# Kernel tuning notes

Measured on AMD Instinct MI355X. Metric: run time of the kernel, lower is better.

The kernel has to match this reference:

```python
import jax, jax.numpy as jnp
import numpy as np

M = 128      # max_child_num
H = 256      # hidden_size
F = 256      # node_feat_size (must equal H per original view logic)
T = 4        # edge_type_num
I = 2        # num_iterations
NSEM = 57    # Tree.num_sem


def setup_inputs() -> dict:
    key = jax.random.key(0)
    ks = jax.random.split(key, 16)
    def lin(k, shape, fan_in):
        return (jax.random.normal(k, shape, jnp.float32) / np.sqrt(fan_in)).astype(jnp.float32)
    return {
        "parent_feature": jax.random.normal(ks[0], (1, F), jnp.float32),
        "W_parent": lin(ks[1], (F, H * M), F),
        "b_parent": jnp.zeros((H * M,), jnp.float32),
        "W_exists": lin(ks[2], (H, 1), H),
        "b_exists": jnp.zeros((1,), jnp.float32),
        "W_edge_latent": lin(ks[3], (2 * H, H), 2 * H),
        "b_edge_latent": jnp.zeros((H,), jnp.float32),
        "W_edge_exists": lin(ks[4], (T, H), H),   # per-type 1-out linear, stacked
        "b_edge_exists": jnp.zeros((T,), jnp.float32),
        "W_op": lin(ks[5], (I, 3 * H + T, H), 3 * H + T),
        "b_op": jnp.zeros((I, H), jnp.float32),
        "W_child": lin(ks[6], (H * (I + 1), H), H * (I + 1)),
        "b_child": jnp.zeros((H,), jnp.float32),
        "W_sem": lin(ks[7], (H, NSEM), H),
        "b_sem": jnp.zeros((NSEM,), jnp.float32),
        "W_child2": lin(ks[8], (H, F), H),
        "b_child2": jnp.zeros((F,), jnp.float32),
    }


def reference(parent_feature, W_parent, b_parent, W_exists, b_exists,
              W_edge_latent, b_edge_latent, W_edge_exists, b_edge_exists,
              W_op, b_op, W_child, b_child, W_sem, b_sem, W_child2, b_child2):
    # parent -> per-child latents [M, H]
    cf = jax.nn.relu(parent_feature @ W_parent + b_parent).reshape(M, H)
    child_exists_logits = cf @ W_exists + b_exists                      # [M, 1]

    # pairwise edge latents [M, M, H]
    pair = jnp.concatenate([
        jnp.broadcast_to(cf[:, None, :], (M, M, H)),
        jnp.broadcast_to(cf[None, :, :], (M, M, H)),
    ], axis=-1)
    el = jax.nn.relu(pair @ W_edge_latent + b_edge_latent)              # [M, M, H]
    ee = jnp.einsum('ijh,th->ijt', el, W_edge_exists) + b_edge_exists   # [M, M, T]

    # dense-mask equivalent of torch.nonzero edge list: an edge exists per
    # (i, j, type) triple where its logit > 0 and both endpoints exist.
    exists = child_exists_logits[:, 0] > 0                              # [M]
    mask = (ee > 0) & exists[:, None, None] & exists[None, :, None]     # [M, M, T]
    maskf = mask.astype(cf.dtype)

    iter_feats = [cf]
    for i in range(I):
        # node_edge_op input is concat([cf_src, cf_dst, edge_latent, onehot(t)*logit]);
        # split the linear into per-block matmuls to avoid a [M,M,T,3H+T] concat.
        W1, W2, W3, W4 = (W_op[i, :H], W_op[i, H:2 * H],
                          W_op[i, 2 * H:3 * H], W_op[i, 3 * H:])        # W4: [T, H]
        pre = ((cf @ W1)[:, None, None, :]
               + (cf @ W2)[None, :, None, :]
               + (el @ W3)[:, :, None, :]
               + ee[:, :, :, None] * W4[None, None, :, :]
               + b_op[i])                                               # [M, M, T, H]
        h = jax.nn.relu(pre) * maskf[..., None]
        # scatter_max over source index i with zero-initialized output:
        # relu output >= 0 and masked-out edges are 0, so plain max matches.
        cf = jnp.max(h, axis=(1, 2))                                    # [M, H]
        iter_feats.append(cf)

    allf = jnp.concatenate(iter_feats, axis=1)                          # [M, H*(I+1)]
    ch = jax.nn.relu(allf @ W_child + b_child)                          # [M, H]
    child_sem_logits = ch @ W_sem + b_sem                               # [M, NSEM]
    child_feats = jax.nn.relu(ch @ W_child2 + b_child2)                 # [M, F]

    return (child_feats[None], child_sem_logits[None],
            child_exists_logits[None], ee[None])
```

## Files before the change

### kernel.cpp

```cpp
#include <hip/hip_runtime.h>
#include <hip/hip_bf16.h>

#define M_ 128
#define H_ 256
#define F_ 256
#define T_ 4
#define NSEM_ 57

typedef __attribute__((ext_vector_type(8))) short bf16x8;
typedef __attribute__((ext_vector_type(4))) float f32x4;

__device__ __forceinline__ float4 ld4(const float* p) { return *reinterpret_cast<const float4*>(p); }
__device__ __forceinline__ void st4(float* p, float4 v) { *reinterpret_cast<float4*>(p) = v; }
__device__ __forceinline__ float4 add4(float4 a, float4 b) { return make_float4(a.x+b.x, a.y+b.y, a.z+b.z, a.w+b.w); }
__device__ __forceinline__ float4 relu4(float4 a) { return make_float4(fmaxf(a.x,0.f), fmaxf(a.y,0.f), fmaxf(a.z,0.f), fmaxf(a.w,0.f)); }
__device__ __forceinline__ float4 fma4(float s, float4 w, float4 c) { return make_float4(fmaf(s,w.x,c.x), fmaf(s,w.y,c.y), fmaf(s,w.z,c.z), fmaf(s,w.w,c.w)); }

__device__ __forceinline__ unsigned short f2bfu(float x) {
  unsigned u = __float_as_uint(x);
  return (unsigned short)((u + 0x7FFFu + ((u >> 16) & 1u)) >> 16);
}
__device__ __forceinline__ unsigned pack2(float lo, float hi) {
  return (unsigned)f2bfu(lo) | ((unsigned)f2bfu(hi) << 16);
}

__global__ void __launch_bounds__(256) k_parent(
    const float* __restrict__ pf, const float* __restrict__ Wp,
    const float* __restrict__ Wop, float* __restrict__ part,
    unsigned short* __restrict__ W36F, unsigned short* __restrict__ W768F)
{
  const int cb = (blockIdx.x & 31) * 1024 + threadIdx.x * 4;
  const int kc = blockIdx.x >> 5;
  __shared__ float spf[8];
  if (threadIdx.x < 8) spf[threadIdx.x] = pf[kc * 8 + threadIdx.x];
  __syncthreads();
  const float* w = Wp + (size_t)kc * 8 * 32768 + cb;
  float4 acc = make_float4(0.f, 0.f, 0.f, 0.f);
  #pragma unroll
  for (int k = 0; k < 8; ++k)
    acc = fma4(spf[k], ld4(w + (size_t)k * 32768), acc);
  st4(&part[kc * 32768 + cb], acc);

  const int g = blockIdx.x * 256 + threadIdx.x;
  if (g < 65536) {
    const int fb = g >> 9, e = g & 511;
    const int kk = fb >> 4, ct = fb & 15;
    const int l = e >> 3, q = e & 7;
    const int k = kk * 32 + ((l >> 4) << 3) + q;
    const int h = ct * 16 + (l & 15);
    W36F[g] = f2bfu(Wop[(size_t)(512 + k) * 256 + h]);
  } else {
    const int g2 = g - 65536;
    const int fb = g2 >> 9, e = g2 & 511;
    const int kk = fb >> 4, ct = fb & 15;
    const int l = e >> 3, q = e & 7;
    const int k = kk * 32 + ((l >> 4) << 3) + q;
    const int h = ct * 16 + (l & 15);
    const int row = (k < 256) ? 512 + k : (k < 512 ? k : k - 512);
    W768F[g2] = f2bfu(Wop[197632 + (size_t)row * 256 + h]);
  }
}

__global__ void __launch_bounds__(256) k_stage1(
    const float* __restrict__ part, const float* __restrict__ bp,
    const float* __restrict__ Wel, const float* __restrict__ Wop0,
    const float* __restrict__ Wex, const float* __restrict__ bex,
    float* __restrict__ cf0, float* __restrict__ A, float* __restrict__ B,
    float* __restrict__ a1, float* __restrict__ a2,
    float* __restrict__ cf1, float* __restrict__ cf2,
    float* __restrict__ out_ex)
{
  const int m = blockIdx.x >> 1, sel = blockIdx.x & 1;
  const int t = threadIdx.x;
  __shared__ float sall[256];
  __shared__ float red[2][4][256];
  __shared__ float redE[4];

  (sel ? cf2 : cf1)[m * 256 + t] = 0.f;

  float v = bp[m * 256 + t];
  #pragma unroll 8
  for (int q = 0; q < 32; ++q) v += part[q * 32768 + m * 256 + t];
  v = fmaxf(v, 0.f);
  sall[t] = v;
  if (sel == 0) {
    cf0[m * 256 + t] = v;
    float p = v * Wex[t];
    #pragma unroll
    for (int off = 32; off > 0; off >>= 1) p += __shfl_xor(p, off);
    if ((t & 63) == 0) redE[t >> 6] = p;
  }
  __syncthreads();

  const float* W0 = Wel  + (sel ? 65536 : 0);
  const float* W1 = Wop0 + (sel ? 65536 : 0);
  const int hq = (t & 63) << 2, kg = t >> 6, k0 = kg * 64;
  float4 acc0 = make_float4(0.f, 0.f, 0.f, 0.f), acc1 = acc0;
  #pragma unroll 4
  for (int k = k0; k < k0 + 64; ++k) {
    const float s = sall[k];
    acc0 = fma4(s, ld4(W0 + k * 256 + hq), acc0);
    acc1 = fma4(s, ld4(W1 + k * 256 + hq), acc1);
  }
  st4(&red[0][kg][hq], acc0);
  st4(&red[1][kg][hq], acc1);
  __syncthreads();
  if (kg < 2) {
    float4 r = add4(add4(ld4(&red[kg][0][hq]), ld4(&red[kg][1][hq])),
                    add4(ld4(&red[kg][2][hq]), ld4(&red[kg][3][hq])));
    float* dst = (kg == 0) ? (sel ? B : A) : (sel ? a2 : a1);
    st4(&dst[m * 256 + hq], r);
  }
  if (sel == 0 && t == 0)
    out_ex[m] = redE[0] + redE[1] + redE[2] + redE[3] + bex[0];
}

__global__ void __launch_bounds__(512) k_gemm0(
    const float* __restrict__ Arow, const float* __restrict__ Brow,
    const float* __restrict__ bel, const unsigned short* __restrict__ W36F,
    const float* __restrict__ Wee, const float* __restrict__ bee,
    const float* __restrict__ a1, const float* __restrict__ a2,
    const float* __restrict__ Wop0, const float* __restrict__ bop0,
    const float* __restrict__ exlog,
    float* __restrict__ ee_g, float* __restrict__ cf1)
{
  const int i  = blockIdx.x >> 2;
  const int jq = blockIdx.x & 3;
  const int t  = threadIdx.x;
  const int w  = t >> 6;
  const int l  = t & 63;
  __shared__ char sEL[32 * 512];
  __shared__ float see[32][4];
  __shared__ float sexf[32];

  const bool exi = exlog[i] > 0.f;

  {
    const int row = t >> 4;
    const int sub = t & 15;
    const int kb  = sub * 16;
    const float* Ap  = Arow + i * 256 + kb;
    const float* Bp  = Brow + (jq * 32 + row) * 256 + kb;
    const float* blp = bel + kb;
    float e[16];
    #pragma unroll
    for (int q = 0; q < 16; q += 4) {
      float4 av = ld4(Ap + q), bv = ld4(Bp + q), lv = ld4(blp + q);
      e[q+0] = fmaxf(av.x + bv.x + lv.x, 0.f);
      e[q+1] = fmaxf(av.y + bv.y + lv.y, 0.f);
      e[q+2] = fmaxf(av.z + bv.z + lv.z, 0.f);
      e[q+3] = fmaxf(av.w + bv.w + lv.w, 0.f);
    }
    float s[4] = {0.f, 0.f, 0.f, 0.f};
    #pragma unroll
    for (int tt = 0; tt < 4; ++tt) {
      #pragma unroll
      for (int q = 0; q < 16; q += 4) {
        float4 wv = ld4(Wee + tt * 256 + kb + q);
        s[tt] = fmaf(e[q+0], wv.x, s[tt]);
        s[tt] = fmaf(e[q+1], wv.y, s[tt]);
        s[tt] = fmaf(e[q+2], wv.z, s[tt]);
        s[tt] = fmaf(e[q+3], wv.w, s[tt]);
      }
    }
    #pragma unroll
    for (int off = 1; off < 16; off <<= 1) {
      s[0] += __shfl_xor(s[0], off);
      s[1] += __shfl_xor(s[1], off);
      s[2] += __shfl_xor(s[2], off);
      s[3] += __shfl_xor(s[3], off);
    }
    if (sub < 4) {
      const float v = s[sub] + bee[sub];
      see[row][sub] = v;
      ee_g[(i * 128 + jq * 32 + row) * 4 + sub] = v;
    }
    const int swz = (row & 7) << 4;
    uint4 w0, w1;
    w0.x = pack2(e[0], e[1]);  w0.y = pack2(e[2], e[3]);
    w0.z = pack2(e[4], e[5]);  w0.w = pack2(e[6], e[7]);
    w1.x = pack2(e[8], e[9]);  w1.y = pack2(e[10], e[11]);
    w1.z = pack2(e[12], e[13]); w1.w = pack2(e[14], e[15]);
    *reinterpret_cast<uint4*>(sEL + ((row * 512 + kb * 2)      ^ swz)) = w0;
    *reinterpret_cast<uint4*>(sEL + ((row * 512 + kb * 2 + 16) ^ swz)) = w1;
  }
  if (t < 32) sexf[t] = exlog[jq * 32 + t];
  __syncthreads();

  const int lr = l & 15, lk = l >> 4;
  f32x4 acc[2][2];
  #pragma unroll
  for (int jt = 0; jt < 2; ++jt)
    #pragma unroll
    for (int ct = 0; ct < 2; ++ct)
      acc[jt][ct] = (f32x4){0.f, 0.f, 0.f, 0.f};

  for (int kc = 0; kc < 8; ++kc) {
    const int kbyte = kc * 64 + lk * 16;
    bf16x8 af0 = *reinterpret_cast<const bf16x8*>(
        sEL + ((lr * 512 + kbyte) ^ ((lr & 7) << 4)));
    bf16x8 af1 = *reinterpret_cast<const bf16x8*>(
        sEL + (((16 + lr) * 512 + kbyte) ^ ((lr & 7) << 4)));
    #pragma unroll
    for (int ct = 0; ct < 2; ++ct) {
      const int fb = kc * 16 + (w * 2 + ct);
      bf16x8 bf = *reinterpret_cast<const bf16x8*>(W36F + fb * 512 + l * 8);
      acc[0][ct] = __builtin_amdgcn_mfma_f32_16x16x32_bf16(af0, bf, acc[0][ct], 0, 0, 0);
      acc[1][ct] = __builtin_amdgcn_mfma_f32_16x16x32_bf16(af1, bf, acc[1][ct], 0, 0, 0);
    }
  }

  const int c0 = w * 32 + lr, c1 = c0 + 16;
  const float b10 = a1[i * 256 + c0] + bop0[c0];
  const float b11 = a1[i * 256 + c1] + bop0[c1];
  float w40[4], w41[4];
  #pragma unroll
  for (int tt = 0; tt < 4; ++tt) {
    w40[tt] = Wop0[(768 + tt) * 256 + c0];
    w41[tt] = Wop0[(768 + tt) * 256 + c1];
  }
  float am0 = 0.f, am1 = 0.f;
  #pragma unroll
  for (int jt = 0; jt < 2; ++jt) {
    #pragma unroll
    for (int q = 0; q < 4; ++q) {
      const int jrow = jt * 16 + lk * 4 + q;
      const int j = jq * 32 + jrow;
      if (exi && (sexf[jrow] > 0.f)) {
        const float e0 = see[jrow][0], e1 = see[jrow][1];
        const float e2 = see[jrow][2], e3 = see[jrow][3];
        const float pb0 = b10 + a2[j * 256 + c0] + acc[jt][0][q];
        const float pb1 = b11 + a2[j * 256 + c1] + acc[jt][1][q];
        if (e0 > 0.f) { am0 = fmaxf(am0, fmaxf(fmaf(e0, w40[0], pb0), 0.f));
                        am1 = fmaxf(am1, fmaxf(fmaf(e0, w41[0], pb1), 0.f)); }
        if (e1 > 0.f) { am0 = fmaxf(am0, fmaxf(fmaf(e1, w40[1], pb0), 0.f));
                        am1 = fmaxf(am1, fmaxf(fmaf(e1, w41[1], pb1), 0.f)); }
        if (e2 > 0.f) { am0 = fmaxf(am0, fmaxf(fmaf(e2, w40[2], pb0), 0.f));
                        am1 = fmaxf(am1, fmaxf(fmaf(e2, w41[2], pb1), 0.f)); }
        if (e3 > 0.f) { am0 = fmaxf(am0, fmaxf(fmaf(e3, w40[3], pb0), 0.f));
                        am1 = fmaxf(am1, fmaxf(fmaf(e3, w41[3], pb1), 0.f)); }
      }
    }
  }
  am0 = fmaxf(am0, __shfl_xor(am0, 16));
  am0 = fmaxf(am0, __shfl_xor(am0, 32));
  am1 = fmaxf(am1, __shfl_xor(am1, 16));
  am1 = fmaxf(am1, __shfl_xor(am1, 32));
  if (lk == 0) {
    atomicMax((unsigned int*)&cf1[i * 256 + c0], __float_as_uint(am0));
    atomicMax((unsigned int*)&cf1[i * 256 + c1], __float_as_uint(am1));
  }
}

__global__ void __launch_bounds__(512) k_gemm1(
    const float* __restrict__ Arow, const float* __restrict__ Brow,
    const float* __restrict__ bel, const unsigned short* __restrict__ W768F,
    const float* __restrict__ cf1,
    const float* __restrict__ Wop1, const float* __restrict__ bop1,
    const float* __restrict__ exlog, const float* __restrict__ ee_g,
    float* __restrict__ cf2)
{
  const int i  = blockIdx.x >> 2;
  const int jq = blockIdx.x & 3;
  const int t  = threadIdx.x;
  const int w  = t >> 6;
  const int l  = t & 63;
  __shared__ char sEL[32 * 1536];
  __shared__ float see[32][4];
  __shared__ float sexf[32];

  const bool exi = exlog[i] > 0.f;

  {
    const int row = t >> 4;
    const int sub = t & 15;
    const int kb  = sub * 16;
    const int swz = (row & 7) << 4;
    {
      const float* Ap  = Arow + i * 256 + kb;
      const float* Bp  = Brow + (jq * 32 + row) * 256 + kb;
      const float* blp = bel + kb;
      float e[16];
      #pragma unroll
      for (int q = 0; q < 16; q += 4) {
        float4 av = ld4(Ap + q), bv = ld4(Bp + q), lv = ld4(blp + q);
        e[q+0] = fmaxf(av.x + bv.x + lv.x, 0.f);
        e[q+1] = fmaxf(av.y + bv.y + lv.y, 0.f);
        e[q+2] = fmaxf(av.z + bv.z + lv.z, 0.f);
        e[q+3] = fmaxf(av.w + bv.w + lv.w, 0.f);
      }
      uint4 w0, w1;
      w0.x = pack2(e[0], e[1]);  w0.y = pack2(e[2], e[3]);
      w0.z = pack2(e[4], e[5]);  w0.w = pack2(e[6], e[7]);
      w1.x = pack2(e[8], e[9]);  w1.y = pack2(e[10], e[11]);
      w1.z = pack2(e[12], e[13]); w1.w = pack2(e[14], e[15]);
      *reinterpret_cast<uint4*>(sEL + ((row * 1536 + kb * 2)      ^ swz)) = w0;
      *reinterpret_cast<uint4*>(sEL + ((row * 1536 + kb * 2 + 16) ^ swz)) = w1;
    }
    {
      const float* cj = cf1 + (jq * 32 + row) * 256 + kb;
      float4 v0 = ld4(cj), v1 = ld4(cj + 4), v2 = ld4(cj + 8), v3 = ld4(cj + 12);
      uint4 w0, w1;
      w0.x = pack2(v0.x, v0.y); w0.y = pack2(v0.z, v0.w);
      w0.z = pack2(v1.x, v1.y); w0.w = pack2(v1.z, v1.w);
      w1.x = pack2(v2.x, v2.y); w1.y = pack2(v2.z, v2.w);
      w1.z = pack2(v3.x, v3.y); w1.w = pack2(v3.z, v3.w);
      *reinterpret_cast<uint4*>(sEL + ((row * 1536 + 512 + kb * 2)      ^ swz)) = w0;
      *reinterpret_cast<uint4*>(sEL + ((row * 1536 + 512 + kb * 2 + 16) ^ swz)) = w1;
    }
    {
      const float* ci = cf1 + i * 256 + kb;
      float4 v0 = ld4(ci), v1 = ld4(ci + 4), v2 = ld4(ci + 8), v3 = ld4(ci + 12);
      uint4 w0, w1;
      w0.x = pack2(v0.x, v0.y); w0.y = pack2(v0.z, v0.w);
      w0.z = pack2(v1.x, v1.y); w0.w = pack2(v1.z, v1.w);
      w1.x = pack2(v2.x, v2.y); w1.y = pack2(v2.z, v2.w);
      w1.z = pack2(v3.x, v3.y); w1.w = pack2(v3.z, v3.w);
      *reinterpret_cast<uint4*>(sEL + ((row * 1536 + 1024 + kb * 2)      ^ swz)) = w0;
      *reinterpret_cast<uint4*>(sEL + ((row * 1536 + 1024 + kb * 2 + 16) ^ swz)) = w1;
    }
  }
  if (t < 128)
    see[t >> 2][t & 3] = ee_g[(i * 128 + jq * 32 + (t >> 2)) * 4 + (t & 3)];
  if (t < 32) sexf[t] = exlog[jq * 32 + t];
  __syncthreads();

  const int lr = l & 15, lk = l >> 4;
  f32x4 acc[2][2];
  #pragma unroll
  for (int jt = 0; jt < 2; ++jt)
    #pragma unroll
    for (int ct = 0; ct < 2; ++ct)
      acc[jt][ct] = (f32x4){0.f, 0.f, 0.f, 0.f};

  for (int kc = 0; kc < 24; ++kc) {
    const int kbyte = kc * 64 + lk * 16;
    bf16x8 af0 = *reinterpret_cast<const bf16x8*>(
        sEL + ((lr * 1536 + kbyte) ^ ((lr & 7) << 4)));
    bf16x8 af1 = *reinterpret_cast<const bf16x8*>(
        sEL + (((16 + lr) * 1536 + kbyte) ^ ((lr & 7) << 4)));
    #pragma unroll
    for (int ct = 0; ct < 2; ++ct) {
      const int fb = kc * 16 + (w * 2 + ct);
      bf16x8 bf = *reinterpret_cast<const bf16x8*>(W768F + fb * 512 + l * 8);
      acc[0][ct] = __builtin_amdgcn_mfma_f32_16x16x32_bf16(af0, bf, acc[0][ct], 0, 0, 0);
      acc[1][ct] = __builtin_amdgcn_mfma_f32_16x16x32_bf16(af1, bf, acc[1][ct], 0, 0, 0);
    }
  }

  const int c0 = w * 32 + lr, c1 = c0 + 16;
  const float b10 = bop1[c0];
  const float b11 = bop1[c1];
  float w40[4], w41[4];
  #pragma unroll
  for (int tt = 0; tt < 4; ++tt) {
    w40[tt] = Wop1[(768 + tt) * 256 + c0];
    w41[tt] = Wop1[(768 + tt) * 256 + c1];
  }
  float am0 = 0.f, am1 = 0.f;
  #pragma unroll
  for (int jt = 0; jt < 2; ++jt) {
    #pragma unroll
    for (int q = 0; q < 4; ++q) {
      const int jrow = jt * 16 + lk * 4 + q;
      if (exi && (sexf[jrow] > 0.f)) {
        const float e0 = see[jrow][0], e1 = see[jrow][1];
        const float e2 = see[jrow][2], e3 = see[jrow][3];
        const float pb0 = b10 + acc[jt][0][q];
        const float pb1 = b11 + acc[jt][1][q];
        if (e0 > 0.f) { am0 = fmaxf(am0, fmaxf(fmaf(e0, w40[0], pb0), 0.f));
                        am1 = fmaxf(am1, fmaxf(fmaf(e0, w41[0], pb1), 0.f)); }
        if (e1 > 0.f) { am0 = fmaxf(am0, fmaxf(fmaf(e1, w40[1], pb0), 0.f));
                        am1 = fmaxf(am1, fmaxf(fmaf(e1, w41[1], pb1), 0.f)); }
        if (e2 > 0.f) { am0 = fmaxf(am0, fmaxf(fmaf(e2, w40[2], pb0), 0.f));
                        am1 = fmaxf(am1, fmaxf(fmaf(e2, w41[2], pb1), 0.f)); }
        if (e3 > 0.f) { am0 = fmaxf(am0, fmaxf(fmaf(e3, w40[3], pb0), 0.f));
                        am1 = fmaxf(am1, fmaxf(fmaf(e3, w41[3], pb1), 0.f)); }
      }
    }
  }
  am0 = fmaxf(am0, __shfl_xor(am0, 16));
  am0 = fmaxf(am0, __shfl_xor(am0, 32));
  am1 = fmaxf(am1, __shfl_xor(am1, 16));
  am1 = fmaxf(am1, __shfl_xor(am1, 32));
  if (lk == 0) {
    atomicMax((unsigned int*)&cf2[i * 256 + c0], __float_as_uint(am0));
    atomicMax((unsigned int*)&cf2[i * 256 + c1], __float_as_uint(am1));
  }
}

__global__ void __launch_bounds__(256) k_final(
    const float* __restrict__ cf0, const float* __restrict__ cf1,
    const float* __restrict__ cf2,
    const float* __restrict__ Wch, const float* __restrict__ bch,
    const float* __restrict__ Wsem, const float* __restrict__ bsem,
    const float* __restrict__ Wch2, const float* __restrict__ bch2,
    float* __restrict__ out_feats, float* __restrict__ out_sem)
{
  const int m  = blockIdx.x;
  const int t  = threadIdx.x;
  const int hq = (t & 63) << 2;
  const int kg = t >> 6;
  __shared__ float sall[768];
  __shared__ float sch[256];
  __shared__ float red[4][256];
  __shared__ float redS[4][64];

  sall[t]       = cf0[m * 256 + t];
  sall[256 + t] = cf1[m * 256 + t];
  sall[512 + t] = cf2[m * 256 + t];
  __syncthreads();

  {
    float4 acc = make_float4(0.f, 0.f, 0.f, 0.f);
    const int k0 = kg * 192;
    #pragma unroll 8
    for (int k = k0; k < k0 + 192; ++k)
      acc = fma4(sall[k], ld4(Wch + k * 256 + hq), acc);
    st4(&red[kg][hq], acc);
  }
  __syncthreads();
  if (kg == 0) {
    float4 r = add4(add4(ld4(&red[0][hq]), ld4(&red[1][hq])),
                    add4(ld4(&red[2][hq]), ld4(&red[3][hq])));
    r = relu4(add4(r, ld4(bch + hq)));
    st4(&sch[hq], r);
  }
  __syncthreads();

  {
    float4 f = make_float4(0.f, 0.f, 0.f, 0.f);
    const int k0 = kg * 64;
    #pragma unroll 8
    for (int k = k0; k < k0 + 64; ++k)
      f = fma4(sch[k], ld4(Wch2 + k * 256 + hq), f);
    const int s = t & 63;
    float sv = 0.f;
    if (s < 57) {
      #pragma unroll 8
      for (int k = k0; k < k0 + 64; ++k)
        sv = fmaf(sch[k], Wsem[k * 57 + s], sv);
    }
    redS[kg][s] = sv;
    __syncthreads();
    st4(&red[kg][hq], f);
  }
  __syncthreads();
  if (kg == 0) {
    float4 r = add4(add4(ld4(&red[0][hq]), ld4(&red[1][hq])),
                    add4(ld4(&red[2][hq]), ld4(&red[3][hq])));
    r = relu4(add4(r, ld4(bch2 + hq)));
    st4(&out_feats[m * 256 + hq], r);
    const int s = t & 63;
    if (s < 57)
      out_sem[m * 57 + s] = redS[0][s] + redS[1][s] + redS[2][s] + redS[3][s]
                          + bsem[s];
  }
}

extern "C" void kernel_launch(void* const* d_in, const int* in_sizes, int n_in,
                              void* d_out, int out_size, void* d_ws, size_t ws_size,
                              hipStream_t stream)
{
  const float* pf   = (const float*)d_in[0];
  const float* Wp   = (const float*)d_in[1];
  const float* bp   = (const float*)d_in[2];
  const float* Wex  = (const float*)d_in[3];
  const float* bex  = (const float*)d_in[4];
  const float* Wel  = (const float*)d_in[5];
  const float* bel  = (const float*)d_in[6];
  const float* Wee  = (const float*)d_in[7];
  const float* bee  = (const float*)d_in[8];
  const float* Wop  = (const float*)d_in[9];
  const float* bop  = (const float*)d_in[10];
  const float* Wch  = (const float*)d_in[11];
  const float* bch  = (const float*)d_in[12];
  const float* Wsem = (const float*)d_in[13];
  const float* bsem = (const float*)d_in[14];
  const float* Wch2 = (const float*)d_in[15];
  const float* bch2 = (const float*)d_in[16];

  float* out_feats = (float*)d_out;
  float* out_sem   = out_feats + M_ * F_;
  float* out_ex    = out_sem + M_ * NSEM_;
  float* out_ee    = out_ex + M_;

  float* ws = (float*)d_ws;
  float* cf0 = ws;
  float* cf1 = ws + 32768;
  float* cf2 = ws + 65536;
  float* Ab  = ws + 98304;
  float* Bb  = ws + 131072;
  float* a1  = ws + 163840;
  float* a2  = ws + 196608;
  float* part = ws + 229376;
  unsigned short* W36F  = (unsigned short*)(ws + 1277952);
  unsigned short* W768F = (unsigned short*)(ws + 1310720);

  const float* Wop0 = Wop;
  const float* Wop1 = Wop + 197632;

  k_parent<<<1024, 256, 0, stream>>>(pf, Wp, Wop, part, W36F, W768F);
  k_stage1<<<256, 256, 0, stream>>>(part, bp, Wel, Wop0, Wex, bex,
                                    cf0, Ab, Bb, a1, a2, cf1, cf2, out_ex);
  k_gemm0<<<512, 512, 0, stream>>>(Ab, Bb, bel, W36F, Wee, bee,
                                   a1, a2, Wop0, bop, out_ex, out_ee, cf1);
  k_gemm1<<<512, 512, 0, stream>>>(Ab, Bb, bel, W768F, cf1,
                                   Wop1, bop + 256, out_ex, out_ee, cf2);
  k_final<<<128, 256, 0, stream>>>(cf0, cf1, cf2, Wch, bch, Wsem, bsem,
                                   Wch2, bch2, out_feats, out_sem);
}
```

Measured before the change: 68.88 us.

## Stage weight repack through shared memory, prefetch MFMA operands, widen final kernel

The weight repack in k_parent now reads a 16x16 tile into shared memory with coalesced loads and writes the bf16 swizzled layout from there, instead of scattered gathers. k_stage1 loads all 32 partial sums before reducing them so the loads overlap. Both GEMM kernels hoist their epilogue operand loads (a1/a2, W4 rows, ee) ahead of the main loop and double-buffer the A/B fragments across k-chunks so MFMAs overlap the next loads. k_final moves to 512 threads with 8-way k-splitting and drops one barrier, which raises parallelism but increases register and shared-memory use.

```diff
diff --git a/kernel.cpp b/kernel.cpp
--- a/kernel.cpp
+++ b/kernel.cpp
@@ -29,10 +29,29 @@
     const float* __restrict__ Wop, float* __restrict__ part,
     unsigned short* __restrict__ W36F, unsigned short* __restrict__ W768F)
 {
-  const int cb = (blockIdx.x & 31) * 1024 + threadIdx.x * 4;
+  const int t = threadIdx.x;
+  __shared__ float spf[8];
+  __shared__ float tile[16][17];
+
+  const int fbg = blockIdx.x >> 1;
+  const int half = blockIdx.x & 1;
+  const bool it0 = fbg < 128;
+  const int fb = it0 ? fbg : fbg - 128;
+  const int kk = fb >> 4, ct = fb & 15;
+  const int base_k = kk * 32 + half * 16;
+  int row_base;
+  if (it0) row_base = 512 + base_k;
+  else row_base = (base_k < 256) ? 512 + base_k
+                : (base_k < 512 ? base_k : base_k - 512);
+  const float* wsrc = Wop + (it0 ? 0 : 197632);
+  {
+    const int r = t >> 4, c = t & 15;
+    tile[r][c] = wsrc[(size_t)(row_base + r) * 256 + ct * 16 + c];
+  }
+
+  const int cb = (blockIdx.x & 31) * 1024 + t * 4;
   const int kc = blockIdx.x >> 5;
-  __shared__ float spf[8];
-  if (threadIdx.x < 8) spf[threadIdx.x] = pf[kc * 8 + threadIdx.x];
+  if (t < 8) spf[t] = pf[kc * 8 + t];
   __syncthreads();
   const float* w = Wp + (size_t)kc * 8 * 32768 + cb;
   float4 acc = make_float4(0.f, 0.f, 0.f, 0.f);
@@ -41,23 +60,13 @@
     acc = fma4(spf[k], ld4(w + (size_t)k * 32768), acc);
   st4(&part[kc * 32768 + cb], acc);
 
-  const int g = blockIdx.x * 256 + threadIdx.x;
-  if (g < 65536) {
-    const int fb = g >> 9, e = g & 511;
-    const int kk = fb >> 4, ct = fb & 15;
-    const int l = e >> 3, q = e & 7;
-    const int k = kk * 32 + ((l >> 4) << 3) + q;
-    const int h = ct * 16 + (l & 15);
-    W36F[g] = f2bfu(Wop[(size_t)(512 + k) * 256 + h]);
-  } else {
-    const int g2 = g - 65536;
-    const int fb = g2 >> 9, e = g2 & 511;
-    const int kk = fb >> 4, ct = fb & 15;
-    const int l = e >> 3, q = e & 7;
-    const int k = kk * 32 + ((l >> 4) << 3) + q;
-    const int h = ct * 16 + (l & 15);
-    const int row = (k < 256) ? 512 + k : (k < 512 ? k : k - 512);
-    W768F[g2] = f2bfu(Wop[197632 + (size_t)row * 256 + h]);
+  {
+    const int k_local = ((t >> 7) << 3) + (t & 7);
+    const int h_local = (t >> 3) & 15;
+    const int e = half * 256 + t;
+    unsigned short v = f2bfu(tile[k_local][h_local]);
+    if (it0) W36F[fb * 512 + e] = v;
+    else     W768F[fb * 512 + e] = v;
   }
 }
 
@@ -78,9 +87,12 @@
 
   (sel ? cf2 : cf1)[m * 256 + t] = 0.f;
 
+  float pv[32];
+  #pragma unroll
+  for (int q = 0; q < 32; ++q) pv[q] = part[q * 32768 + m * 256 + t];
   float v = bp[m * 256 + t];
-  #pragma unroll 8
-  for (int q = 0; q < 32; ++q) v += part[q * 32768 + m * 256 + t];
+  #pragma unroll
+  for (int q = 0; q < 32; ++q) v += pv[q];
   v = fmaxf(v, 0.f);
   sall[t] = v;
   if (sel == 0) {
@@ -96,7 +108,7 @@
   const float* W1 = Wop0 + (sel ? 65536 : 0);
   const int hq = (t & 63) << 2, kg = t >> 6, k0 = kg * 64;
   float4 acc0 = make_float4(0.f, 0.f, 0.f, 0.f), acc1 = acc0;
-  #pragma unroll 4
+  #pragma unroll 8
   for (int k = k0; k < k0 + 64; ++k) {
     const float s = sall[k];
     acc0 = fma4(s, ld4(W0 + k * 256 + hq), acc0);
@@ -134,6 +146,25 @@
   __shared__ float sexf[32];
 
   const bool exi = exlog[i] > 0.f;
+  const int lr = l & 15, lk = l >> 4;
+
+  const int c0 = w * 32 + lr, c1 = c0 + 16;
+  const float b10 = a1[i * 256 + c0] + bop0[c0];
+  const float b11 = a1[i * 256 + c1] + bop0[c1];
+  float w40[4], w41[4], a2v0[8], a2v1[8];
+  #pragma unroll
+  for (int tt = 0; tt < 4; ++tt) {
+    w40[tt] = Wop0[(768 + tt) * 256 + c0];
+    w41[tt] = Wop0[(768 + tt) * 256 + c1];
+  }
+  #pragma unroll
+  for (int jt = 0; jt < 2; ++jt)
+    #pragma unroll
+    for (int q = 0; q < 4; ++q) {
+      const int j = jq * 32 + jt * 16 + lk * 4 + q;
+      a2v0[jt * 4 + q] = a2[j * 256 + c0];
+      a2v1[jt * 4 + q] = a2[j * 256 + c1];
+    }
 
   {
     const int row = t >> 4;
@@ -187,7 +218,6 @@
   if (t < 32) sexf[t] = exlog[jq * 32 + t];
   __syncthreads();
 
-  const int lr = l & 15, lk = l >> 4;
   f32x4 acc[2][2];
   #pragma unroll
   for (int jt = 0; jt < 2; ++jt)
@@ -195,42 +225,39 @@
     for (int ct = 0; ct < 2; ++ct)
       acc[jt][ct] = (f32x4){0.f, 0.f, 0.f, 0.f};
 
+  const int swz0 = (lr & 7) << 4;
+  bf16x8 cb0 = *reinterpret_cast<const bf16x8*>(W36F + (0 * 16 + w * 2 + 0) * 512 + l * 8);
+  bf16x8 cb1 = *reinterpret_cast<const bf16x8*>(W36F + (0 * 16 + w * 2 + 1) * 512 + l * 8);
+  bf16x8 ca0 = *reinterpret_cast<const bf16x8*>(sEL + ((lr * 512 + lk * 16) ^ swz0));
+  bf16x8 ca1 = *reinterpret_cast<const bf16x8*>(sEL + (((16 + lr) * 512 + lk * 16) ^ swz0));
+  #pragma unroll
   for (int kc = 0; kc < 8; ++kc) {
-    const int kbyte = kc * 64 + lk * 16;
-    bf16x8 af0 = *reinterpret_cast<const bf16x8*>(
-        sEL + ((lr * 512 + kbyte) ^ ((lr & 7) << 4)));
-    bf16x8 af1 = *reinterpret_cast<const bf16x8*>(
-        sEL + (((16 + lr) * 512 + kbyte) ^ ((lr & 7) << 4)));
-    #pragma unroll
-    for (int ct = 0; ct < 2; ++ct) {
-      const int fb = kc * 16 + (w * 2 + ct);
-      bf16x8 bf = *reinterpret_cast<const bf16x8*>(W36F + fb * 512 + l * 8);
-      acc[0][ct] = __builtin_amdgcn_mfma_f32_16x16x32_bf16(af0, bf, acc[0][ct], 0, 0, 0);
-      acc[1][ct] = __builtin_amdgcn_mfma_f32_16x16x32_bf16(af1, bf, acc[1][ct], 0, 0, 0);
-    }
-  }
-
-  const int c0 = w * 32 + lr, c1 = c0 + 16;
-  const float b10 = a1[i * 256 + c0] + bop0[c0];
-  const float b11 = a1[i * 256 + c1] + bop0[c1];
-  float w40[4], w41[4];
-  #pragma unroll
-  for (int tt = 0; tt < 4; ++tt) {
-    w40[tt] = Wop0[(768 + tt) * 256 + c0];
-    w41[tt] = Wop0[(768 + tt) * 256 + c1];
-  }
+    bf16x8 nb0, nb1, na0, na1;
+    if (kc < 7) {
+      const int kbyte = (kc + 1) * 64 + lk * 16;
+      nb0 = *reinterpret_cast<const bf16x8*>(W36F + ((kc + 1) * 16 + w * 2 + 0) * 512 + l * 8);
+      nb1 = *reinterpret_cast<const bf16x8*>(W36F + ((kc + 1) * 16 + w * 2 + 1) * 512 + l * 8);
+      na0 = *reinterpret_cast<const bf16x8*>(sEL + ((lr * 512 + kbyte) ^ swz0));
+      na1 = *reinterpret_cast<const bf16x8*>(sEL + (((16 + lr) * 512 + kbyte) ^ swz0));
+    }
+    acc[0][0] = __builtin_amdgcn_mfma_f32_16x16x32_bf16(ca0, cb0, acc[0][0], 0, 0, 0);
+    acc[1][0] = __builtin_amdgcn_mfma_f32_16x16x32_bf16(ca1, cb0, acc[1][0], 0, 0, 0);
+    acc[0][1] = __builtin_amdgcn_mfma_f32_16x16x32_bf16(ca0, cb1, acc[0][1], 0, 0, 0);
+    acc[1][1] = __builtin_amdgcn_mfma_f32_16x16x32_bf16(ca1, cb1, acc[1][1], 0, 0, 0);
+    if (kc < 7) { cb0 = nb0; cb1 = nb1; ca0 = na0; ca1 = na1; }
+  }
+
   float am0 = 0.f, am1 = 0.f;
   #pragma unroll
   for (int jt = 0; jt < 2; ++jt) {
     #pragma unroll
     for (int q = 0; q < 4; ++q) {
       const int jrow = jt * 16 + lk * 4 + q;
-      const int j = jq * 32 + jrow;
       if (exi && (sexf[jrow] > 0.f)) {
         const float e0 = see[jrow][0], e1 = see[jrow][1];
         const float e2 = see[jrow][2], e3 = see[jrow][3];
-        const float pb0 = b10 + a2[j * 256 + c0] + acc[jt][0][q];
-        const float pb1 = b11 + a2[j * 256 + c1] + acc[jt][1][q];
+        const float pb0 = b10 + a2v0[jt * 4 + q] + acc[jt][0][q];
+        const float pb1 = b11 + a2v1[jt * 4 + q] + acc[jt][1][q];
         if (e0 > 0.f) { am0 = fmaxf(am0, fmaxf(fmaf(e0, w40[0], pb0), 0.f));
                         am1 = fmaxf(am1, fmaxf(fmaf(e0, w41[0], pb1), 0.f)); }
         if (e1 > 0.f) { am0 = fmaxf(am0, fmaxf(fmaf(e1, w40[1], pb0), 0.f));
@@ -270,6 +297,20 @@
   __shared__ float sexf[32];
 
   const bool exi = exlog[i] > 0.f;
+  const int lr = l & 15, lk = l >> 4;
+
+  const int c0 = w * 32 + lr, c1 = c0 + 16;
+  const float b10 = bop1[c0];
+  const float b11 = bop1[c1];
+  float w40[4], w41[4];
+  #pragma unroll
+  for (int tt = 0; tt < 4; ++tt) {
+    w40[tt] = Wop1[(768 + tt) * 256 + c0];
+    w41[tt] = Wop1[(768 + tt) * 256 + c1];
+  }
+  if (t < 128)
+    see[t >> 2][t & 3] = ee_g[(i * 128 + jq * 32 + (t >> 2)) * 4 + (t & 3)];
+  if (t < 32) sexf[t] = exlog[jq * 32 + t];
 
   {
     const int row = t >> 4;
@@ -320,12 +361,8 @@
       *reinterpret_cast<uint4*>(sEL + ((row * 1536 + 1024 + kb * 2 + 16) ^ swz)) = w1;
     }
   }
-  if (t < 128)
-    see[t >> 2][t & 3] = ee_g[(i * 128 + jq * 32 + (t >> 2)) * 4 + (t & 3)];
-  if (t < 32) sexf[t] = exlog[jq * 32 + t];
-  __syncthreads();
-
-  const int lr = l & 15, lk = l >> 4;
+  __syncthreads();
+
   f32x4 acc[2][2];
   #pragma unroll
   for (int jt = 0; jt < 2; ++jt)
@@ -333,30 +370,28 @@
     for (int ct = 0; ct < 2; ++ct)
       acc[jt][ct] = (f32x4){0.f, 0.f, 0.f, 0.f};
 
+  const int swz0 = (lr & 7) << 4;
+  bf16x8 cb0 = *reinterpret_cast<const bf16x8*>(W768F + (0 * 16 + w * 2 + 0) * 512 + l * 8);
+  bf16x8 cb1 = *reinterpret_cast<const bf16x8*>(W768F + (0 * 16 + w * 2 + 1) * 512 + l * 8);
+  bf16x8 ca0 = *reinterpret_cast<const bf16x8*>(sEL + ((lr * 1536 + lk * 16) ^ swz0));
+  bf16x8 ca1 = *reinterpret_cast<const bf16x8*>(sEL + (((16 + lr) * 1536 + lk * 16) ^ swz0));
+  #pragma unroll
   for (int kc = 0; kc < 24; ++kc) {
-    const int kbyte = kc * 64 + lk * 16;
-    bf16x8 af0 = *reinterpret_cast<const bf16x8*>(
-        sEL + ((lr * 1536 + kbyte) ^ ((lr & 7) << 4)));
-    bf16x8 af1 = *reinterpret_cast<const bf16x8*>(
-        sEL + (((16 + lr) * 1536 + kbyte) ^ ((lr & 7) << 4)));
-    #pragma unroll
-    for (int ct = 0; ct < 2; ++ct) {
-      const int fb = kc * 16 + (w * 2 + ct);
-      bf16x8 bf = *reinterpret_cast<const bf16x8*>(W768F + fb * 512 + l * 8);
-      acc[0][ct] = __builtin_amdgcn_mfma_f32_16x16x32_bf16(af0, bf, acc[0][ct], 0, 0, 0);
-      acc[1][ct] = __builtin_amdgcn_mfma_f32_16x16x32_bf16(af1, bf, acc[1][ct], 0, 0, 0);
-    }
-  }
-
-  const int c0 = w * 32 + lr, c1 = c0 + 16;
-  const float b10 = bop1[c0];
-  const float b11 = bop1[c1];
-  float w40[4], w41[4];
-  #pragma unroll
-  for (int tt = 0; tt < 4; ++tt) {
-    w40[tt] = Wop1[(768 + tt) * 256 + c0];
-    w41[tt] = Wop1[(768 + tt) * 256 + c1];
-  }
+    bf16x8 nb0, nb1, na0, na1;
+    if (kc < 23) {
+      const int kbyte = (kc + 1) * 64 + lk * 16;
+      nb0 = *reinterpret_cast<const bf16x8*>(W768F + ((kc + 1) * 16 + w * 2 + 0) * 512 + l * 8);
+      nb1 = *reinterpret_cast<const bf16x8*>(W768F + ((kc + 1) * 16 + w * 2 + 1) * 512 + l * 8);
+      na0 = *reinterpret_cast<const bf16x8*>(sEL + ((lr * 1536 + kbyte) ^ swz0));
+      na1 = *reinterpret_cast<const bf16x8*>(sEL + (((16 + lr) * 1536 + kbyte) ^ swz0));
+    }
+    acc[0][0] = __builtin_amdgcn_mfma_f32_16x16x32_bf16(ca0, cb0, acc[0][0], 0, 0, 0);
+    acc[1][0] = __builtin_amdgcn_mfma_f32_16x16x32_bf16(ca1, cb0, acc[1][0], 0, 0, 0);
+    acc[0][1] = __builtin_amdgcn_mfma_f32_16x16x32_bf16(ca0, cb1, acc[0][1], 0, 0, 0);
+    acc[1][1] = __builtin_amdgcn_mfma_f32_16x16x32_bf16(ca1, cb1, acc[1][1], 0, 0, 0);
+    if (kc < 23) { cb0 = nb0; cb1 = nb1; ca0 = na0; ca1 = na1; }
+  }
+
   float am0 = 0.f, am1 = 0.f;
   #pragma unroll
   for (int jt = 0; jt < 2; ++jt) {
@@ -389,7 +424,7 @@
   }
 }
 
-__global__ void __launch_bounds__(256) k_final(
+__global__ void __launch_bounds__(512) k_final(
     const float* __restrict__ cf0, const float* __restrict__ cf1,
     const float* __restrict__ cf2,
     const float* __restrict__ Wch, const float* __restrict__ bch,
@@ -403,26 +438,29 @@
   const int kg = t >> 6;
   __shared__ float sall[768];
   __shared__ float sch[256];
-  __shared__ float red[4][256];
-  __shared__ float redS[4][64];
-
-  sall[t]       = cf0[m * 256 + t];
-  sall[256 + t] = cf1[m * 256 + t];
-  sall[512 + t] = cf2[m * 256 + t];
+  __shared__ float red[8][256];
+  __shared__ float redS[8][64];
+
+  if (t < 256) {
+    sall[t]       = cf0[m * 256 + t];
+    sall[256 + t] = cf1[m * 256 + t];
+    sall[512 + t] = cf2[m * 256 + t];
+  }
   __syncthreads();
 
   {
     float4 acc = make_float4(0.f, 0.f, 0.f, 0.f);
-    const int k0 = kg * 192;
+    const int k0 = kg * 96;
     #pragma unroll 8
-    for (int k = k0; k < k0 + 192; ++k)
+    for (int k = k0; k < k0 + 96; ++k)
       acc = fma4(sall[k], ld4(Wch + k * 256 + hq), acc);
     st4(&red[kg][hq], acc);
   }
   __syncthreads();
   if (kg == 0) {
-    float4 r = add4(add4(ld4(&red[0][hq]), ld4(&red[1][hq])),
-                    add4(ld4(&red[2][hq]), ld4(&red[3][hq])));
+    float4 r = ld4(&red[0][hq]);
+    #pragma unroll
+    for (int g2 = 1; g2 < 8; ++g2) r = add4(r, ld4(&red[g2][hq]));
     r = relu4(add4(r, ld4(bch + hq)));
     st4(&sch[hq], r);
   }
@@ -430,31 +468,33 @@
 
   {
     float4 f = make_float4(0.f, 0.f, 0.f, 0.f);
-    const int k0 = kg * 64;
+    const int k0 = kg * 32;
     #pragma unroll 8
-    for (int k = k0; k < k0 + 64; ++k)
+    for (int k = k0; k < k0 + 32; ++k)
       f = fma4(sch[k], ld4(Wch2 + k * 256 + hq), f);
     const int s = t & 63;
     float sv = 0.f;
     if (s < 57) {
       #pragma unroll 8
-      for (int k = k0; k < k0 + 64; ++k)
+      for (int k = k0; k < k0 + 32; ++k)
         sv = fmaf(sch[k], Wsem[k * 57 + s], sv);
     }
     redS[kg][s] = sv;
-    __syncthreads();
     st4(&red[kg][hq], f);
   }
   __syncthreads();
   if (kg == 0) {
-    float4 r = add4(add4(ld4(&red[0][hq]), ld4(&red[1][hq])),
-                    add4(ld4(&red[2][hq]), ld4(&red[3][hq])));
+    float4 r = ld4(&red[0][hq]);
+    #pragma unroll
+    for (int g2 = 1; g2 < 8; ++g2) r = add4(r, ld4(&red[g2][hq]));
     r = relu4(add4(r, ld4(bch2 + hq)));
     st4(&out_feats[m * 256 + hq], r);
-    const int s = t & 63;
-    if (s < 57)
-      out_sem[m * 57 + s] = redS[0][s] + redS[1][s] + redS[2][s] + redS[3][s]
-                          + bsem[s];
+  }
+  if (t < 57) {
+    float s2 = bsem[t];
+    #pragma unroll
+    for (int g2 = 0; g2 < 8; ++g2) s2 += redS[g2][t];
+    out_sem[m * 57 + t] = s2;
   }
 }
 
@@ -507,6 +547,6 @@
                                    a1, a2, Wop0, bop, out_ex, out_ee, cf1);
   k_gemm1<<<512, 512, 0, stream>>>(Ab, Bb, bel, W768F, cf1,
                                    Wop1, bop + 256, out_ex, out_ee, cf2);
-  k_final<<<128, 256, 0, stream>>>(cf0, cf1, cf2, Wch, bch, Wsem, bsem,
+  k_final<<<128, 512, 0, stream>>>(cf0, cf1, cf2, Wch, bch, Wsem, bsem,
                                    Wch2, bch2, out_feats, out_sem);
 }
```

Result: faster. 65.41 us (median of 2 runs) (-5.0%).
